# Performance work log

Hardware: AMD Instinct MI355X
Metric: run time of the kernel (lower is better)

Reference implementation:

```python
import jax, jax.numpy as jnp
import numpy as np

N_NODES = 20000
N_EDGES = 200000
N_GRAPHS = 128
IN_DIM = 256
HID = 512
HEADS = 8
C = HID // HEADS  # 64
LAT = 256
NEG_SLOPE = 0.2
BN_EPS = 1e-5


def setup_inputs() -> dict:
    key = jax.random.key(0)
    ks = jax.random.split(key, 24)
    n = lambda k, s, sc=0.05: jax.random.normal(k, s, jnp.float32) * sc
    return {
        'x': jax.random.normal(ks[0], (N_NODES, IN_DIM), jnp.float32),
        'edge_index': jax.random.randint(ks[1], (2, N_EDGES), 0, N_NODES, jnp.int32),
        'batch': jnp.sort(jax.random.randint(ks[2], (N_NODES,), 0, N_GRAPHS, jnp.int32)),
        'Wl0': n(ks[3], (IN_DIM, HID)), 'bl0': n(ks[4], (HID,)),
        'Wr0': n(ks[5], (IN_DIM, HID)), 'br0': n(ks[6], (HID,)),
        'att0': n(ks[7], (HEADS, C)), 'bias0': n(ks[8], (HID,)),
        'Wl1': n(ks[9], (HID, HID)), 'bl1': n(ks[10], (HID,)),
        'Wr1': n(ks[11], (HID, HID)), 'br1': n(ks[12], (HID,)),
        'att1': n(ks[13], (HEADS, C)), 'bias1': n(ks[14], (HID,)),
        'bn_gamma': jnp.ones((HID,), jnp.float32),
        'bn_beta': jnp.zeros((HID,), jnp.float32),
        'bn_mean': n(ks[15], (HID,)),
        'bn_var': jax.random.uniform(ks[16], (HID,), jnp.float32, 0.5, 1.5),
        'Wfc': n(ks[17], (HID, LAT)), 'bfc': n(ks[18], (LAT,)),
    }


def gatv2_layer(x, src, dst, Wl, bl, Wr, br, att, bias):
    # x: [N, F]; returns [N, HEADS*C]. GATv2: e = a . LeakyReLU(Wl x_src + Wr x_dst)
    xl = (x @ Wl + bl).reshape(-1, HEADS, C)  # source transform [N,H,C]
    xr = (x @ Wr + br).reshape(-1, HEADS, C)  # target transform [N,H,C]
    feat = jax.nn.leaky_relu(xl[src] + xr[dst], NEG_SLOPE)     # [E,H,C]
    logits = jnp.einsum('ehc,hc->eh', feat, att)               # [E,H]
    # segment softmax over incoming edges of each target node
    m = jax.ops.segment_max(logits, dst, num_segments=N_NODES)  # [N,H]
    p = jnp.exp(logits - m[dst])
    denom = jax.ops.segment_sum(p, dst, num_segments=N_NODES)   # [N,H]
    alpha = p / (denom[dst] + 1e-16)                            # [E,H]
    msg = xl[src] * alpha[:, :, None]                           # [E,H,C]
    out = jax.ops.segment_sum(msg, dst, num_segments=N_NODES)   # [N,H,C]
    return out.reshape(-1, HEADS * C) + bias


def reference(x, edge_index, batch, Wl0, bl0, Wr0, br0, att0, bias0,
              Wl1, bl1, Wr1, br1, att1, bias1,
              bn_gamma, bn_beta, bn_mean, bn_var, Wfc, bfc):
    src, dst = edge_index[0], edge_index[1]
    # layer 0 + ELU (dropout is identity in eval mode)
    h = jax.nn.elu(gatv2_layer(x, src, dst, Wl0, bl0, Wr0, br0, att0, bias0))
    # layer 1 + ELU
    h = jax.nn.elu(gatv2_layer(h, src, dst, Wl1, bl1, Wr1, br1, att1, bias1))
    # global add pool over graphs
    g = jax.ops.segment_sum(h, batch, num_segments=N_GRAPHS)  # [G, HID]
    # BatchNorm1d (eval mode: running stats)
    g = (g - bn_mean) * jax.lax.rsqrt(bn_var + BN_EPS) * bn_gamma + bn_beta
    return g @ Wfc + bfc  # [G, LAT]
```

## Files before the change

kernel.cpp:

```cpp
#include <hip/hip_runtime.h>
#include <hip/hip_bf16.h>
#include <cstdint>

#define NN 20000
#define NE 200000
#define NG 128
#define HID 512
#define XLR_W 1024

typedef __attribute__((ext_vector_type(4))) float f32x4;
typedef __attribute__((ext_vector_type(8))) short s16x8;

__device__ __forceinline__ float bf2f(unsigned short u) {
  union { unsigned int i; float f; } v; v.i = ((unsigned int)u) << 16; return v.f;
}
__device__ __forceinline__ unsigned short f2bf(float f) {
  union { float f; unsigned int i; } v; v.f = f;
  unsigned int i = v.i + 0x7FFFu + ((v.i >> 16) & 1u);
  return (unsigned short)(i >> 16);
}
__device__ __forceinline__ float asf(unsigned int u) {
  union { unsigned int i; float f; } v; v.i = u; return v.f;
}

#define GLOAD16(gp, lp)                                                        \
  __builtin_amdgcn_global_load_lds(                                            \
      (const __attribute__((address_space(1))) unsigned int*)(gp),             \
      (__attribute__((address_space(3))) unsigned int*)(lp), 16, 0, 0)

__global__ __launch_bounds__(256) void k_prep(const float* __restrict__ x,
                                              unsigned short* __restrict__ xb,
                                              const float* __restrict__ Wl0, const float* __restrict__ bl0,
                                              const float* __restrict__ Wr0, const float* __restrict__ br0,
                                              unsigned short* __restrict__ wt0, float* __restrict__ bcat0,
                                              const float* __restrict__ Wl1, const float* __restrict__ bl1,
                                              const float* __restrict__ Wr1, const float* __restrict__ br1,
                                              unsigned short* __restrict__ wt1, float* __restrict__ bcat1,
                                              int* __restrict__ deg,
                                              unsigned long long* __restrict__ st) {
  int b = blockIdx.x, t = threadIdx.x;
  if (b < 79) {
    int i = b * 256 + t;
    if (i < NN) deg[i] = 0;
  } else if (b == 79) {
    if (t < 32) st[t] = 0ULL;
  } else if (b < 5080) {
    int i = (b - 80) * 256 + t;
    float4 v = ((const float4*)x)[i];
    ushort4 o;
    o.x = f2bf(v.x); o.y = f2bf(v.y); o.z = f2bf(v.z); o.w = f2bf(v.w);
    ((ushort4*)xb)[i] = o;
  } else if (b < 6104) {
    int id = (b - 5080) * 256 + t;
    int nrow = id >> 8, k = id & 255;
    float v = (nrow < HID) ? Wl0[k * HID + nrow] : Wr0[k * HID + (nrow - HID)];
    wt0[id] = f2bf(v);
    if (id < XLR_W) bcat0[id] = (id < HID) ? bl0[id] : br0[id - HID];
  } else {
    int id = (b - 6104) * 256 + t;
    int nrow = id >> 9, k = id & 511;
    float v = (nrow < HID) ? Wl1[k * HID + nrow] : Wr1[k * HID + (nrow - HID)];
    wt1[id] = f2bf(v);
    if (id < XLR_W) bcat1[id] = (id < HID) ? bl1[id] : br1[id - HID];
  }
}

__global__ __launch_bounds__(1024) void k_scan(const int* __restrict__ deg,
                                               int* __restrict__ offs,
                                               int* __restrict__ woff,
                                               unsigned long long* __restrict__ st,
                                               int n) {
  __shared__ int wsum[16];
  __shared__ int sexcl;
  int t = threadIdx.x;
  int wid = t >> 6, lane = t & 63;
  int i = blockIdx.x * 1024 + t;
  int v = (i < n) ? deg[i] : 0;
  int s = v;
#pragma unroll
  for (int off = 1; off < 64; off <<= 1) {
    int x = __shfl_up(s, off, 64);
    if (lane >= off) s += x;
  }
  if (lane == 63) wsum[wid] = s;
  __syncthreads();
  if (wid == 0) {
    int ws = (lane < 16) ? wsum[lane] : 0;
#pragma unroll
    for (int off = 1; off < 16; off <<= 1) {
      int x = __shfl_up(ws, off, 64);
      if (lane >= off) ws += x;
    }
    if (lane < 16) wsum[lane] = ws;
  }
  __syncthreads();
  int ex = s - v + (wid ? wsum[wid - 1] : 0);
  int bt = wsum[15];
  if (t == 1023) {
    int excl = 0;
    int bid = blockIdx.x;
    if (bid > 0) {
      unsigned long long val;
      do { val = atomicAdd(&st[bid - 1], 0ULL); } while (!(val >> 63));
      excl = (int)(val & 0xFFFFFFFFULL);
    }
    atomicExch(&st[blockIdx.x], (1ULL << 63) | (unsigned long long)(unsigned)(excl + bt));
    sexcl = excl;
    if (bid == (int)gridDim.x - 1) offs[n] = excl + bt;
  }
  __syncthreads();
  int base = sexcl;
  if (i < n) {
    int val = ex + base;
    offs[i] = val;
    woff[i] = val;
  }
}

__global__ void k_scatter(const int* __restrict__ src, const int* __restrict__ dst,
                          int* __restrict__ woff, int* __restrict__ src_s, int E) {
  int i = blockIdx.x * blockDim.x + threadIdx.x;
  if (i < E) {
    int d = dst[i];
    int pos = atomicAdd(&woff[d], 1);
    src_s[pos] = src[i];
  }
}

#define BM 128
#define BN 128
#define PLN 4096

__global__ __launch_bounds__(256) void k_gemm(const unsigned short* __restrict__ A,
                                              const unsigned short* __restrict__ Bt,
                                              const float* __restrict__ bias,
                                              unsigned short* __restrict__ C,
                                              int M, int N, int K, int nby,
                                              const int* __restrict__ hdst,
                                              int* __restrict__ deg,
                                              int gemmBlocks, int histN) {
  __shared__ __align__(16) unsigned short As[2 * PLN];
  __shared__ __align__(16) unsigned short Bs[2 * PLN];
  int L = blockIdx.x;
  if (L >= gemmBlocks) {
    int i = (L - gemmBlocks) * 256 + threadIdx.x;
    if (i < histN) atomicAdd(&deg[hdst[i]], 1);
    return;
  }
  int by = (L & 7) | ((L >> 6) << 3);
  int bx = (L >> 3) & 7;
  if (by >= nby) return;
  int m0 = by * BM, n0 = bx * BN;

  int t = threadIdx.x;
  int wave = t >> 6, lane = t & 63;
  int wm = (wave >> 1) * 64, wn = (wave & 1) * 64;
  int ml = lane & 15, mq = lane >> 4;
  int lr = lane >> 2;
  int qg = (lane & 3) ^ ((lane >> 3) & 3);
  int lq = qg * 8;

  f32x4 acc[4][4];
#pragma unroll
  for (int i = 0; i < 4; i++)
#pragma unroll
    for (int j = 0; j < 4; j++) acc[i][j] = (f32x4)0.0f;

  const unsigned short* gA[4];
  const unsigned short* gB[4];
  unsigned short* lA[4];
  unsigned short* lB[4];
#pragma unroll
  for (int p = 0; p < 2; p++)
#pragma unroll
    for (int h = 0; h < 2; h++) {
      int idx = p * 2 + h;
      int arow = m0 + wave * 32 + h * 16 + lr; if (arow > M - 1) arow = M - 1;
      gA[idx] = A + (size_t)arow * K + p * 32 + lq;
      gB[idx] = Bt + (size_t)(n0 + wave * 32 + h * 16 + lr) * K + p * 32 + lq;
      lA[idx] = &As[p * PLN + (wave * 32 + h * 16) * 32];
      lB[idx] = &Bs[p * PLN + (wave * 32 + h * 16) * 32];
    }

  int qr = (mq ^ ((ml >> 1) & 3)) * 8;

  int T = K >> 6;
  for (int tt = 0; tt < T; tt++) {
#pragma unroll
    for (int idx = 0; idx < 4; idx++) {
      GLOAD16(gA[idx], lA[idx]);
      GLOAD16(gB[idx], lB[idx]);
      gA[idx] += 64; gB[idx] += 64;
    }
    __syncthreads();
#pragma unroll
    for (int kq = 0; kq < 2; kq++) {
      s16x8 af[4], bfr[4];
#pragma unroll
      for (int i = 0; i < 4; i++)
        af[i] = *(const s16x8*)(&As[kq * PLN + (wm + i * 16 + ml) * 32 + qr]);
#pragma unroll
      for (int j = 0; j < 4; j++)
        bfr[j] = *(const s16x8*)(&Bs[kq * PLN + (wn + j * 16 + ml) * 32 + qr]);
#pragma unroll
      for (int i = 0; i < 4; i++)
#pragma unroll
        for (int j = 0; j < 4; j++)
          acc[i][j] = __builtin_amdgcn_mfma_f32_16x16x32_bf16(af[i], bfr[j], acc[i][j], 0, 0, 0);
    }
    __syncthreads();
  }

#pragma unroll
  for (int i = 0; i < 4; i++) {
#pragma unroll
    for (int j = 0; j < 4; j++) {
      int col = n0 + wn + j * 16 + ml;
      float bcol = bias[col];
#pragma unroll
      for (int r = 0; r < 4; r++) {
        int row = m0 + wm + i * 16 + mq * 4 + r;
        if (row < M) C[(size_t)row * N + col] = f2bf(acc[i][j][r] + bcol);
      }
    }
  }
}

__global__ __launch_bounds__(256) void k_attn(const unsigned short* __restrict__ xlr,
                                              const float* __restrict__ att,
                                              const int* __restrict__ offs,
                                              const int* __restrict__ src_s,
                                              const float* __restrict__ bias,
                                              unsigned short* __restrict__ hout) {
  __shared__ float red[4][8][68];
  __shared__ float reds[4][8];
  int n = blockIdx.x;
  int wave = threadIdx.x >> 6, lane = threadIdx.x & 63;
  int h = lane >> 3, k = lane & 7;
  int c = h * 64 + k * 8;
  int s0 = offs[n], s1 = offs[n + 1];

  uint4 uxr = *(const uint4*)(xlr + (size_t)n * XLR_W + HID + c);
  float xr[8];
  xr[0] = asf(uxr.x << 16); xr[1] = asf(uxr.x & 0xFFFF0000u);
  xr[2] = asf(uxr.y << 16); xr[3] = asf(uxr.y & 0xFFFF0000u);
  xr[4] = asf(uxr.z << 16); xr[5] = asf(uxr.z & 0xFFFF0000u);
  xr[6] = asf(uxr.w << 16); xr[7] = asf(uxr.w & 0xFFFF0000u);
  float at[8];
  {
    const float4* ap = (const float4*)(att + c);
    float4 a0 = ap[0], a1 = ap[1];
    at[0] = a0.x; at[1] = a0.y; at[2] = a0.z; at[3] = a0.w;
    at[4] = a1.x; at[5] = a1.y; at[6] = a1.z; at[7] = a1.w;
  }

  float acc[8] = {0.f, 0.f, 0.f, 0.f, 0.f, 0.f, 0.f, 0.f};
  float sum = 0.0f;

  int i = s0 + wave;
  uint4 u_cur = make_uint4(0, 0, 0, 0);
  if (i < s1) {
    int s = src_s[i];
    u_cur = *(const uint4*)(xlr + (size_t)s * XLR_W + c);
  }
  int nx = i + 4;
  for (; i < s1; i += 4) {
    uint4 u = u_cur;
    if (nx < s1) {
      int s = src_s[nx];
      u_cur = *(const uint4*)(xlr + (size_t)s * XLR_W + c);
    }
    nx += 4;

    float xl[8];
    xl[0] = asf(u.x << 16); xl[1] = asf(u.x & 0xFFFF0000u);
    xl[2] = asf(u.y << 16); xl[3] = asf(u.y & 0xFFFF0000u);
    xl[4] = asf(u.z << 16); xl[5] = asf(u.z & 0xFFFF0000u);
    xl[6] = asf(u.w << 16); xl[7] = asf(u.w & 0xFFFF0000u);

    float l = 0.0f;
#pragma unroll
    for (int j = 0; j < 8; j++) {
      float v = xl[j] + xr[j];
      v = fmaf(0.4f, fabsf(v), 0.6f * v);
      l = fmaf(v, at[j], l);
    }
    l += __shfl_xor(l, 1, 64);
    l += __shfl_xor(l, 2, 64);
    l += __shfl_xor(l, 4, 64);

    float p = __expf(l);
    sum += p;
#pragma unroll
    for (int j = 0; j < 8; j++) acc[j] = fmaf(p, xl[j], acc[j]);
  }

#pragma unroll
  for (int j = 0; j < 8; j++) red[wave][h][k * 8 + j] = acc[j];
  if (k == 0) reds[wave][h] = sum;
  __syncthreads();

  int t = threadIdx.x;
  int cc = t * 2;
  int hh = cc >> 6, off = cc & 63;
  float a0 = red[0][hh][off] + red[1][hh][off] + red[2][hh][off] + red[3][hh][off];
  float a1 = red[0][hh][off + 1] + red[1][hh][off + 1] + red[2][hh][off + 1] + red[3][hh][off + 1];
  float sm = reds[0][hh] + reds[1][hh] + reds[2][hh] + reds[3][hh];
  float di = 1.0f / (sm + 1e-16f);
  float o_a = a0 * di + bias[cc];
  float o_b = a1 * di + bias[cc + 1];
  o_a = o_a > 0.0f ? o_a : (__expf(o_a) - 1.0f);
  o_b = o_b > 0.0f ? o_b : (__expf(o_b) - 1.0f);
  unsigned int up = (unsigned int)f2bf(o_a) | ((unsigned int)f2bf(o_b) << 16);
  *(unsigned int*)(hout + (size_t)n * HID + cc) = up;
}

__device__ __forceinline__ int lower_bound(const int* __restrict__ a, int n, int key) {
  int lo = 0, hi = n;
  while (lo < hi) { int mid = (lo + hi) >> 1; if (a[mid] < key) lo = mid + 1; else hi = mid; }
  return lo;
}

__global__ __launch_bounds__(256) void k_pool(const unsigned short* __restrict__ h,
                                              const int* __restrict__ batch,
                                              float* __restrict__ part) {
  int g = blockIdx.x, p = blockIdx.y, t = threadIdx.x;
  int start = lower_bound(batch, NN, g);
  int end = lower_bound(batch, NN, g + 1);
  int cntq = (end - start + 3) >> 2;
  int lo = start + p * cntq;
  int hi = lo + cntq; if (hi > end) hi = end;
  int c = t * 2;
  float a0 = 0.0f, a1 = 0.0f;
  for (int n = lo; n < hi; n++) {
    unsigned int u = *(const unsigned int*)(h + (size_t)n * HID + c);
    a0 += asf(u << 16);
    a1 += asf(u & 0xFFFF0000u);
  }
  float* dstp = part + ((size_t)g * 4 + p) * HID + c;
  dstp[0] = a0;
  dstp[1] = a1;
}

__global__ __launch_bounds__(256) void k_fc(const float* __restrict__ part,
                                            const float* __restrict__ gamma,
                                            const float* __restrict__ beta,
                                            const float* __restrict__ mean,
                                            const float* __restrict__ var,
                                            const float* __restrict__ Wfc,
                                            const float* __restrict__ bfc,
                                            float* __restrict__ out) {
  __shared__ float xsm[512];
  int g = blockIdx.x, t = threadIdx.x;
  for (int c = t; c < HID; c += 256) {
    float s = part[((size_t)g * 4 + 0) * HID + c] + part[((size_t)g * 4 + 1) * HID + c]
            + part[((size_t)g * 4 + 2) * HID + c] + part[((size_t)g * 4 + 3) * HID + c];
    xsm[c] = (s - mean[c]) * rsqrtf(var[c] + 1e-5f) * gamma[c] + beta[c];
  }
  __syncthreads();
  float acc = bfc[t];
#pragma unroll 8
  for (int k = 0; k < 512; k++) acc += xsm[k] * Wfc[k * 256 + t];
  out[g * 256 + t] = acc;
}

extern "C" void kernel_launch(void* const* d_in, const int* in_sizes, int n_in,
                              void* d_out, int out_size, void* d_ws, size_t ws_size,
                              hipStream_t stream) {
  const float* x     = (const float*)d_in[0];
  const int* ei      = (const int*)d_in[1];
  const int* batch   = (const int*)d_in[2];
  const float* Wl0   = (const float*)d_in[3];
  const float* bl0   = (const float*)d_in[4];
  const float* Wr0   = (const float*)d_in[5];
  const float* br0   = (const float*)d_in[6];
  const float* att0  = (const float*)d_in[7];
  const float* bias0 = (const float*)d_in[8];
  const float* Wl1   = (const float*)d_in[9];
  const float* bl1   = (const float*)d_in[10];
  const float* Wr1   = (const float*)d_in[11];
  const float* br1   = (const float*)d_in[12];
  const float* att1  = (const float*)d_in[13];
  const float* bias1 = (const float*)d_in[14];
  const float* gamma = (const float*)d_in[15];
  const float* beta  = (const float*)d_in[16];
  const float* mean  = (const float*)d_in[17];
  const float* var   = (const float*)d_in[18];
  const float* Wfc   = (const float*)d_in[19];
  const float* bfc   = (const float*)d_in[20];

  const int* src = ei;
  const int* dst = ei + NE;

  char* w = (char*)d_ws;
  size_t off = 0;
  auto alloc = [&](size_t bytes) -> void* {
    void* p = w + off;
    off += (bytes + 255) & ~(size_t)255;
    return p;
  };
  int* deg                 = (int*)alloc((size_t)NN * 4);
  int* offs                = (int*)alloc((size_t)(NN + 1) * 4);
  int* woff                = (int*)alloc((size_t)NN * 4);
  int* src_s               = (int*)alloc((size_t)NE * 4);
  unsigned long long* st   = (unsigned long long*)alloc((size_t)32 * 8);
  unsigned short* xb       = (unsigned short*)alloc((size_t)NN * 256 * 2);
  unsigned short* xlr      = (unsigned short*)alloc((size_t)NN * XLR_W * 2);
  unsigned short* hb       = (unsigned short*)alloc((size_t)NN * HID * 2);
  unsigned short* wt0      = (unsigned short*)alloc((size_t)XLR_W * 256 * 2);
  unsigned short* wt1      = (unsigned short*)alloc((size_t)XLR_W * HID * 2);
  float* bcat0             = (float*)alloc((size_t)XLR_W * 4);
  float* bcat1             = (float*)alloc((size_t)XLR_W * 4);
  float* part              = (float*)alloc((size_t)NG * 4 * HID * 4);

  const int NB   = (NN + 1023) / 1024;
  const int NBY  = (NN + BM - 1) / BM;
  const int GRID = 64 * ((NBY + 7) / 8);
  const int HB   = (NE + 255) / 256;

  k_prep<<<8152, 256, 0, stream>>>(x, xb, Wl0, bl0, Wr0, br0, wt0, bcat0,
                                   Wl1, bl1, Wr1, br1, wt1, bcat1, deg, st);
  k_gemm<<<GRID + HB, 256, 0, stream>>>(xb, wt0, bcat0, xlr, NN, XLR_W, 256, NBY,
                                        dst, deg, GRID, NE);
  k_scan<<<NB, 1024, 0, stream>>>(deg, offs, woff, st, NN);
  k_scatter<<<HB, 256, 0, stream>>>(src, dst, woff, src_s, NE);
  k_attn<<<NN, 256, 0, stream>>>(xlr, att0, offs, src_s, bias0, hb);
  k_gemm<<<GRID, 256, 0, stream>>>(hb, wt1, bcat1, xlr, NN, XLR_W, 512, NBY,
                                   nullptr, nullptr, GRID, 0);
  k_attn<<<NN, 256, 0, stream>>>(xlr, att1, offs, src_s, bias1, hb);
  k_pool<<<dim3(NG, 4), 256, 0, stream>>>(hb, batch, part);
  k_fc<<<NG, 256, 0, stream>>>(part, gamma, beta, mean, var, Wfc, bfc, (float*)d_out);
}
```

Measured before the change: 319.8 us.

## Assign one wavefront per destination node in attention kernel, drop LDS reduction

The attention kernel now maps each wavefront to a single destination node, so one block handles four nodes, instead of splitting a node's edges across four waves and combining them through shared memory. This removes the LDS reduction, the __syncthreads barrier and the per-node block launch overhead. The output is written as 16-byte vector stores. The edge loop becomes serial per wave, with a one-ahead prefetch of the source index and row. This may lengthen latency chains for high-degree nodes and leaves wave-level load imbalance inside a block.

```diff
diff --git a/kernel.cpp b/kernel.cpp
--- a/kernel.cpp
+++ b/kernel.cpp
@@ -232,13 +232,13 @@
                                               const int* __restrict__ src_s,
                                               const float* __restrict__ bias,
                                               unsigned short* __restrict__ hout) {
-  __shared__ float red[4][8][68];
-  __shared__ float reds[4][8];
-  int n = blockIdx.x;
   int wave = threadIdx.x >> 6, lane = threadIdx.x & 63;
+  int n = blockIdx.x * 4 + wave;
+  if (n >= NN) return;
   int h = lane >> 3, k = lane & 7;
   int c = h * 64 + k * 8;
   int s0 = offs[n], s1 = offs[n + 1];
+  int last = s1 - 1;
 
   uint4 uxr = *(const uint4*)(xlr + (size_t)n * XLR_W + HID + c);
   float xr[8];
@@ -257,62 +257,57 @@
   float acc[8] = {0.f, 0.f, 0.f, 0.f, 0.f, 0.f, 0.f, 0.f};
   float sum = 0.0f;
 
-  int i = s0 + wave;
-  uint4 u_cur = make_uint4(0, 0, 0, 0);
-  if (i < s1) {
-    int s = src_s[i];
-    u_cur = *(const uint4*)(xlr + (size_t)s * XLR_W + c);
-  }
-  int nx = i + 4;
-  for (; i < s1; i += 4) {
-    uint4 u = u_cur;
-    if (nx < s1) {
-      int s = src_s[nx];
-      u_cur = *(const uint4*)(xlr + (size_t)s * XLR_W + c);
-    }
-    nx += 4;
-
-    float xl[8];
-    xl[0] = asf(u.x << 16); xl[1] = asf(u.x & 0xFFFF0000u);
-    xl[2] = asf(u.y << 16); xl[3] = asf(u.y & 0xFFFF0000u);
-    xl[4] = asf(u.z << 16); xl[5] = asf(u.z & 0xFFFF0000u);
-    xl[6] = asf(u.w << 16); xl[7] = asf(u.w & 0xFFFF0000u);
-
-    float l = 0.0f;
+  if (s0 <= last) {
+    int sA = src_s[s0];
+    uint4 u_cur = *(const uint4*)(xlr + (size_t)sA * XLR_W + c);
+    int sB = src_s[min(s0 + 1, last)];
+    for (int i = s0; i <= last; i++) {
+      uint4 u = u_cur;
+      u_cur = *(const uint4*)(xlr + (size_t)sB * XLR_W + c);
+      sB = src_s[min(i + 2, last)];
+
+      float xl[8];
+      xl[0] = asf(u.x << 16); xl[1] = asf(u.x & 0xFFFF0000u);
+      xl[2] = asf(u.y << 16); xl[3] = asf(u.y & 0xFFFF0000u);
+      xl[4] = asf(u.z << 16); xl[5] = asf(u.z & 0xFFFF0000u);
+      xl[6] = asf(u.w << 16); xl[7] = asf(u.w & 0xFFFF0000u);
+
+      float l = 0.0f;
+#pragma unroll
+      for (int j = 0; j < 8; j++) {
+        float v = xl[j] + xr[j];
+        v = fmaf(0.4f, fabsf(v), 0.6f * v);
+        l = fmaf(v, at[j], l);
+      }
+      l += __shfl_xor(l, 1, 64);
+      l += __shfl_xor(l, 2, 64);
+      l += __shfl_xor(l, 4, 64);
+
+      float p = __expf(l);
+      sum += p;
+#pragma unroll
+      for (int j = 0; j < 8; j++) acc[j] = fmaf(p, xl[j], acc[j]);
+    }
+  }
+
+  float di = 1.0f / (sum + 1e-16f);
+  float o[8];
+  {
+    const float4* bp = (const float4*)(bias + c);
+    float4 b0 = bp[0], b1 = bp[1];
+    float bb[8] = {b0.x, b0.y, b0.z, b0.w, b1.x, b1.y, b1.z, b1.w};
 #pragma unroll
     for (int j = 0; j < 8; j++) {
-      float v = xl[j] + xr[j];
-      v = fmaf(0.4f, fabsf(v), 0.6f * v);
-      l = fmaf(v, at[j], l);
-    }
-    l += __shfl_xor(l, 1, 64);
-    l += __shfl_xor(l, 2, 64);
-    l += __shfl_xor(l, 4, 64);
-
-    float p = __expf(l);
-    sum += p;
-#pragma unroll
-    for (int j = 0; j < 8; j++) acc[j] = fmaf(p, xl[j], acc[j]);
-  }
-
-#pragma unroll
-  for (int j = 0; j < 8; j++) red[wave][h][k * 8 + j] = acc[j];
-  if (k == 0) reds[wave][h] = sum;
-  __syncthreads();
-
-  int t = threadIdx.x;
-  int cc = t * 2;
-  int hh = cc >> 6, off = cc & 63;
-  float a0 = red[0][hh][off] + red[1][hh][off] + red[2][hh][off] + red[3][hh][off];
-  float a1 = red[0][hh][off + 1] + red[1][hh][off + 1] + red[2][hh][off + 1] + red[3][hh][off + 1];
-  float sm = reds[0][hh] + reds[1][hh] + reds[2][hh] + reds[3][hh];
-  float di = 1.0f / (sm + 1e-16f);
-  float o_a = a0 * di + bias[cc];
-  float o_b = a1 * di + bias[cc + 1];
-  o_a = o_a > 0.0f ? o_a : (__expf(o_a) - 1.0f);
-  o_b = o_b > 0.0f ? o_b : (__expf(o_b) - 1.0f);
-  unsigned int up = (unsigned int)f2bf(o_a) | ((unsigned int)f2bf(o_b) << 16);
-  *(unsigned int*)(hout + (size_t)n * HID + cc) = up;
+      float v = acc[j] * di + bb[j];
+      o[j] = v > 0.0f ? v : (__expf(v) - 1.0f);
+    }
+  }
+  uint4 outp;
+  outp.x = (unsigned int)f2bf(o[0]) | ((unsigned int)f2bf(o[1]) << 16);
+  outp.y = (unsigned int)f2bf(o[2]) | ((unsigned int)f2bf(o[3]) << 16);
+  outp.z = (unsigned int)f2bf(o[4]) | ((unsigned int)f2bf(o[5]) << 16);
+  outp.w = (unsigned int)f2bf(o[6]) | ((unsigned int)f2bf(o[7]) << 16);
+  *(uint4*)(hout + (size_t)n * HID + c) = outp;
 }
 
 __device__ __forceinline__ int lower_bound(const int* __restrict__ a, int n, int key) {
@@ -424,10 +419,10 @@
                                         dst, deg, GRID, NE);
   k_scan<<<NB, 1024, 0, stream>>>(deg, offs, woff, st, NN);
   k_scatter<<<HB, 256, 0, stream>>>(src, dst, woff, src_s, NE);
-  k_attn<<<NN, 256, 0, stream>>>(xlr, att0, offs, src_s, bias0, hb);
+  k_attn<<<(NN + 3) / 4, 256, 0, stream>>>(xlr, att0, offs, src_s, bias0, hb);
   k_gemm<<<GRID, 256, 0, stream>>>(hb, wt1, bcat1, xlr, NN, XLR_W, 512, NBY,
                                    nullptr, nullptr, GRID, 0);
-  k_attn<<<NN, 256, 0, stream>>>(xlr, att1, offs, src_s, bias1, hb);
+  k_attn<<<(NN + 3) / 4, 256, 0, stream>>>(xlr, att1, offs, src_s, bias1, hb);
   k_pool<<<dim3(NG, 4), 256, 0, stream>>>(hb, batch, part);
   k_fc<<<NG, 256, 0, stream>>>(part, gamma, beta, mean, var, Wfc, bfc, (float*)d_out);
 }
```

Measured after the change: 315.3 us. Within noise of the previous version (-1.4%).
